# Optimization experiments

Hardware: AMD Instinct MI355X
Metric: run time of the kernel (lower is better)

The kernel has to match this reference:

```python
import jax, jax.numpy as jnp
import numpy as np

N_QUBITS = 12


def _apply_rx(state, q, theta, n):
    B = state.shape[0]
    left, right = 1 << q, 1 << (n - q - 1)
    s = state.reshape(B, left, 2, right)
    th = jnp.atleast_1d(jnp.asarray(theta)).reshape(-1, 1, 1)  # (B,1,1) or (1,1,1)
    c = jnp.cos(0.5 * th).astype(state.dtype)
    ms = (-1j * jnp.sin(0.5 * th)).astype(state.dtype)
    s0, s1 = s[:, :, 0, :], s[:, :, 1, :]
    new = jnp.stack([c * s0 + ms * s1, ms * s0 + c * s1], axis=2)
    return new.reshape(B, -1)


def _apply_cnot(state, ctrl, tgt, n):
    # flip target amplitudes on the control=1 slab
    B = state.shape[0]
    a, b = min(ctrl, tgt), max(ctrl, tgt)
    shape = (B, 1 << a, 2, 1 << (b - a - 1), 2, 1 << (n - b - 1))
    ax_c = 2 if ctrl == a else 4
    ax_t = 4 if ctrl == a else 2
    s = state.reshape(shape)
    s0 = jnp.take(s, 0, axis=ax_c)
    s1 = jnp.take(s, 1, axis=ax_c)
    ax_t_after = ax_t - 1 if ax_t > ax_c else ax_t
    s1 = jnp.flip(s1, axis=ax_t_after)
    return jnp.stack([s0, s1], axis=ax_c).reshape(B, -1)


def _simulate(x, w):
    # x: (B, n) angles; w: (L, n) angles. Returns (B, n) Pauli-Z expectations.
    B, n = x.shape
    L = w.shape[0]
    state = jnp.zeros((B, 1 << n), jnp.complex64).at[:, 0].set(1.0)
    # angle embedding: RX(x[:, j]) on qubit j
    for j in range(n):
        state = _apply_rx(state, j, x[:, j], n)
    # VQC layers: RX(w[i, j]) then ring of CNOTs
    for i in range(L):
        for j in range(n):
            state = _apply_rx(state, j, w[i, j], n)
        if n == 2:
            state = _apply_cnot(state, 0, 1, n)
        elif n > 2:
            for j in range(n):
                state = _apply_cnot(state, j, (j + 1) % n, n)
    probs = state.real ** 2 + state.imag ** 2  # (B, 2^n)
    exps = []
    for i in range(n):
        p = probs.reshape(B, 1 << i, 2, -1).sum(axis=(1, 3))  # (B, 2)
        exps.append(p[:, 0] - p[:, 1])
    return jnp.stack(exps, axis=-1)


def setup_inputs() -> dict:
    key = jax.random.key(0)
    k1, k2 = jax.random.split(key)
    x = jax.random.normal(k1, (2048, N_QUBITS), dtype=jnp.float32)
    # xavier_normal-ish init for w of shape (num_layers, num_qubits)
    w = jax.random.normal(k2, (2, N_QUBITS), dtype=jnp.float32) * 0.3
    return {"x": x, "w": w}


def reference(x, w):
    return _simulate(x, w)
```

## Files before the change

### kernel.cpp

```cpp
#include <hip/hip_runtime.h>

#define NQ 12
#define NSTATES (1 << NQ)

struct QPlan { unsigned rx2[NQ]; unsigned sgn[NQ]; };

constexpr QPlan make_plan() {
    QPlan P{};
    unsigned grow[NQ] = {}, hcol[NQ] = {};
    for (int j = 0; j < NQ; ++j) { grow[j] = 1u << j; hcol[j] = 1u << j; }
    for (int j = 0; j < NQ; ++j) {
        int cb = NQ - 1 - j, tb = NQ - 1 - ((j + 1) % NQ);
        grow[tb] ^= grow[cb]; hcol[cb] ^= hcol[tb];
    }
    for (int q = 0; q < NQ; ++q) P.rx2[q] = hcol[NQ - 1 - q];
    for (int j = 0; j < NQ; ++j) {
        int cb = NQ - 1 - j, tb = NQ - 1 - ((j + 1) % NQ);
        grow[tb] ^= grow[cb]; hcol[cb] ^= hcol[tb];
    }
    for (int q = 0; q < NQ; ++q) P.sgn[q] = grow[NQ - 1 - q];
    return P;
}
constexpr QPlan QP = make_plan();

__device__ __forceinline__ void rx_pair(float& ur, float& ui, float& vr, float& vi,
                                        float c, float s) {
    float nur = fmaf(c, ur,  s * vi);
    float nui = fmaf(c, ui, -s * vr);
    float nvr = fmaf(c, vr,  s * ui);
    float nvi = fmaf(c, vi, -s * ur);
    ur = nur; ui = nui; vr = nvr; vi = nvi;
}

template <int MLOC>
__device__ __forceinline__ void rx_local(float (&ar)[64], float (&ai)[64], float c, float s) {
    #pragma unroll
    for (int ka = 0; ka < 64; ++ka) {
        const int kb = ka ^ MLOC;
        if (ka < kb) rx_pair(ar[ka], ai[ka], ar[kb], ai[kb], c, s);
    }
}

template <int MLOC, int LM>
__device__ __forceinline__ void rx_shfl(float (&ar)[64], float (&ai)[64], float c, float s) {
    if constexpr (MLOC == 0) {
        #pragma unroll
        for (int k = 0; k < 64; ++k) {
            float pr = __shfl_xor(ar[k], LM, 64);
            float pi = __shfl_xor(ai[k], LM, 64);
            ar[k] = fmaf(c, ar[k],  s * pi);
            ai[k] = fmaf(c, ai[k], -s * pr);
        }
    } else {
        #pragma unroll
        for (int ka = 0; ka < 64; ++ka) {
            const int kb = ka ^ MLOC;
            if (ka < kb) {
                float pra = __shfl_xor(ar[kb], LM, 64);
                float pia = __shfl_xor(ai[kb], LM, 64);
                float prb = __shfl_xor(ar[ka], LM, 64);
                float pib = __shfl_xor(ai[ka], LM, 64);
                ar[ka] = fmaf(c, ar[ka],  s * pia);
                ai[ka] = fmaf(c, ai[ka], -s * pra);
                ar[kb] = fmaf(c, ar[kb],  s * pib);
                ai[kb] = fmaf(c, ai[kb], -s * prb);
            }
        }
    }
}

template <unsigned MASK>
__device__ __forceinline__ void rx_A(float (&ar)[64], float (&ai)[64], float c, float s) {
    constexpr int MLOC = MASK & 63, LM = (MASK >> 6) & 63;
    if constexpr (LM == 0) rx_local<MLOC>(ar, ai, c, s);
    else                   rx_shfl<MLOC, LM>(ar, ai, c, s);
}
template <unsigned MASK>
__device__ __forceinline__ void rx_B(float (&ar)[64], float (&ai)[64], float c, float s) {
    constexpr int MLOC = (MASK >> 6) & 63, LM = MASK & 63;
    if constexpr (LM == 0) rx_local<MLOC>(ar, ai, c, s);
    else                   rx_shfl<MLOC, LM>(ar, ai, c, s);
}

__global__ __launch_bounds__(64, 2) void qsim_fast(
    const float* __restrict__ x, const float* __restrict__ w, float* __restrict__ out)
{
    __shared__ float tbuf[64 * 65];
    const int b = blockIdx.x;
    const int l = threadIdx.x;

    float c0[NQ], s0[NQ], c2[NQ], s2[NQ];
    #pragma unroll
    for (int j = 0; j < NQ; ++j) {
        __sincosf(0.5f * (x[b * NQ + j] + w[j]), &s0[j], &c0[j]);
        __sincosf(0.5f * w[NQ + j],              &s2[j], &c2[j]);
    }

    float ar[64], ai[64];
    {
        float Flo[8], Fhi[8];
        #pragma unroll
        for (int a = 0; a < 8; ++a) {
            Flo[a] = ((a & 1) ? s0[5] : c0[5]) * ((a & 2) ? s0[4] : c0[4]) * ((a & 4) ? s0[3] : c0[3]);
            Fhi[a] = ((a & 1) ? s0[2] : c0[2]) * ((a & 2) ? s0[1] : c0[1]) * ((a & 4) ? s0[0] : c0[0]);
        }
        float Flane = ((l & 1)  ? s0[11] : c0[11]) * ((l & 2)  ? s0[10] : c0[10])
                    * ((l & 4)  ? s0[9]  : c0[9])  * ((l & 8)  ? s0[8]  : c0[8])
                    * ((l & 16) ? s0[7]  : c0[7])  * ((l & 32) ? s0[6]  : c0[6]);
        const int r = __popc(l);
        float rs[4], is[4];
        #pragma unroll
        for (int cc = 0; cc < 4; ++cc) {
            int n2 = (r + cc) & 3;
            rs[cc] = (n2 == 0) ? 1.f : ((n2 == 2) ? -1.f : 0.f);
            is[cc] = (n2 == 1) ? -1.f : ((n2 == 3) ? 1.f : 0.f);
        }
        #pragma unroll
        for (int k = 0; k < 64; ++k) {
            float m = Flane * Fhi[k >> 3] * Flo[k & 7];
            const int cls = __builtin_popcount((unsigned)k) & 3;
            ar[k] = m * rs[cls];
            ai[k] = m * is[cls];
        }
    }

    rx_B<QP.rx2[0]>(ar, ai, c2[0], s2[0]);
    rx_B<QP.rx2[1]>(ar, ai, c2[1], s2[1]);
    rx_B<QP.rx2[2]>(ar, ai, c2[2], s2[2]);
    rx_B<QP.rx2[3]>(ar, ai, c2[3], s2[3]);
    rx_B<QP.rx2[4]>(ar, ai, c2[4], s2[4]);

    #pragma unroll
    for (int k = 0; k < 64; ++k) tbuf[k * 65 + l] = ar[k];
    __syncthreads();
    #pragma unroll
    for (int k = 0; k < 64; ++k) ar[k] = tbuf[l * 65 + k];
    __syncthreads();
    #pragma unroll
    for (int k = 0; k < 64; ++k) tbuf[k * 65 + l] = ai[k];
    __syncthreads();
    #pragma unroll
    for (int k = 0; k < 64; ++k) ai[k] = tbuf[l * 65 + k];

    rx_A<QP.rx2[6]>(ar, ai, c2[6], s2[6]);
    rx_A<QP.rx2[7]>(ar, ai, c2[7], s2[7]);
    rx_A<QP.rx2[8]>(ar, ai, c2[8], s2[8]);
    rx_A<QP.rx2[9]>(ar, ai, c2[9], s2[9]);
    rx_A<QP.rx2[10]>(ar, ai, c2[10], s2[10]);
    rx_A<QP.rx2[5]>(ar, ai, c2[5], s2[5]);
    rx_A<QP.rx2[11]>(ar, ai, c2[11], s2[11]);

    float ex[NQ];
    #pragma unroll
    for (int q = 0; q < NQ; ++q) ex[q] = 0.f;
    #pragma unroll
    for (int k = 0; k < 64; ++k) {
        float p = fmaf(ar[k], ar[k], ai[k] * ai[k]);
        #pragma unroll
        for (int q = 0; q < NQ; ++q) {
            if (__builtin_popcount(QP.sgn[q] & (unsigned)k) & 1) ex[q] -= p;
            else                                                 ex[q] += p;
        }
    }
    #pragma unroll
    for (int q = 0; q < NQ; ++q) {
        float lsgn = (__popc(((QP.sgn[q] >> 6) & 63u) & (unsigned)l) & 1) ? -1.f : 1.f;
        float v = ex[q] * lsgn;
        #pragma unroll
        for (int off = 32; off >= 1; off >>= 1) v += __shfl_xor(v, off, 64);
        ex[q] = v;
    }
    float o = 0.f;
    #pragma unroll
    for (int q = 0; q < NQ; ++q) o = (l == q) ? ex[q] : o;
    if (l < NQ) out[b * NQ + l] = o;
}

__global__ __launch_bounds__(256) void qsim_generic(
    const float* __restrict__ x, const float* __restrict__ w,
    float* __restrict__ out, int L)
{
    __shared__ float re[NSTATES];
    __shared__ float im[NSTATES];
    __shared__ float wsum[4][NQ];
    const int b = blockIdx.x;
    const int t = threadIdx.x;

    for (int i = t; i < NSTATES; i += 256) { re[i] = 0.0f; im[i] = 0.0f; }
    if (t == 0) re[0] = 1.0f;
    __syncthreads();

    auto apply_rx = [&](int q, float theta) {
        const int bit = NQ - 1 - q, mask = 1 << bit;
        const float c = cosf(0.5f * theta), s = sinf(0.5f * theta);
        #pragma unroll
        for (int it = 0; it < NSTATES / 2 / 256; ++it) {
            const int p  = t + it * 256;
            const int i0 = ((p >> bit) << (bit + 1)) | (p & (mask - 1));
            const int i1 = i0 | mask;
            const float a0r = re[i0], a0i = im[i0], a1r = re[i1], a1i = im[i1];
            re[i0] = c * a0r + s * a1i;  im[i0] = c * a0i - s * a1r;
            re[i1] = c * a1r + s * a0i;  im[i1] = c * a1i - s * a0r;
        }
        __syncthreads();
    };
    auto apply_cnot = [&](int ctrl, int tgt) {
        const int cbit = NQ - 1 - ctrl, tbit = NQ - 1 - tgt;
        const int lo = cbit < tbit ? cbit : tbit, hi = cbit < tbit ? tbit : cbit;
        #pragma unroll
        for (int it = 0; it < NSTATES / 4 / 256; ++it) {
            const int p  = t + it * 256;
            const int x1 = ((p  >> lo) << (lo + 1)) | (p  & ((1 << lo) - 1));
            const int x2 = ((x1 >> hi) << (hi + 1)) | (x1 & ((1 << hi) - 1));
            const int ia = x2 | (1 << cbit), ib = ia | (1 << tbit);
            const float tr = re[ia]; re[ia] = re[ib]; re[ib] = tr;
            const float ti = im[ia]; im[ia] = im[ib]; im[ib] = ti;
        }
        __syncthreads();
    };

    for (int j = 0; j < NQ; ++j) apply_rx(j, x[b * NQ + j]);
    for (int l2 = 0; l2 < L; ++l2) {
        for (int j = 0; j < NQ; ++j) apply_rx(j, w[l2 * NQ + j]);
        for (int j = 0; j < NQ; ++j) apply_cnot(j, (j + 1) % NQ);
    }

    float ex[NQ];
    #pragma unroll
    for (int q = 0; q < NQ; ++q) ex[q] = 0.0f;
    #pragma unroll
    for (int it = 0; it < NSTATES / 256; ++it) {
        const int i = t + it * 256;
        const float p = re[i] * re[i] + im[i] * im[i];
        #pragma unroll
        for (int q = 0; q < NQ; ++q) ex[q] += ((i >> (NQ - 1 - q)) & 1) ? -p : p;
    }
    #pragma unroll
    for (int q = 0; q < NQ; ++q) {
        float v = ex[q];
        #pragma unroll
        for (int off = 32; off > 0; off >>= 1) v += __shfl_down(v, off, 64);
        ex[q] = v;
    }
    const int wid = t >> 6, lane = t & 63;
    if (lane == 0) {
        #pragma unroll
        for (int q = 0; q < NQ; ++q) wsum[wid][q] = ex[q];
    }
    __syncthreads();
    if (t < NQ) {
        float v = 0.0f;
        #pragma unroll
        for (int k = 0; k < 4; ++k) v += wsum[k][t];
        out[b * NQ + t] = v;
    }
}

extern "C" void kernel_launch(void* const* d_in, const int* in_sizes, int n_in,
                              void* d_out, int out_size, void* d_ws, size_t ws_size,
                              hipStream_t stream) {
    const float* x = (const float*)d_in[0];
    const float* w = (const float*)d_in[1];
    float* out = (float*)d_out;
    const int B = in_sizes[0] / NQ;
    const int L = in_sizes[1] / NQ;
    if (L == 2) {
        qsim_fast<<<dim3(B), dim3(64), 0, stream>>>(x, w, out);
    } else {
        qsim_generic<<<dim3(B), dim3(256), 0, stream>>>(x, w, out, L);
    }
}
```

Baseline: 70.97 us.

## Factor state into per-thread product and split across 256 threads with fewer gates

Result: faster. 69.23 us (-2.5%).

```diff
diff --git a/kernel.cpp b/kernel.cpp
--- a/kernel.cpp
+++ b/kernel.cpp
@@ -23,157 +23,190 @@
 }
 constexpr QPlan QP = make_plan();
 
-__device__ __forceinline__ void rx_pair(float& ur, float& ui, float& vr, float& vi,
-                                        float c, float s) {
-    float nur = fmaf(c, ur,  s * vi);
-    float nui = fmaf(c, ui, -s * vr);
-    float nvr = fmaf(c, vr,  s * ui);
-    float nvi = fmaf(c, vi, -s * ur);
-    ur = nur; ui = nui; vr = nvr; vi = nvi;
-}
-
-template <int MLOC>
-__device__ __forceinline__ void rx_local(float (&ar)[64], float (&ai)[64], float c, float s) {
-    #pragma unroll
-    for (int ka = 0; ka < 64; ++ka) {
-        const int kb = ka ^ MLOC;
-        if (ka < kb) rx_pair(ar[ka], ai[ka], ar[kb], ai[kb], c, s);
-    }
-}
-
-template <int MLOC, int LM>
-__device__ __forceinline__ void rx_shfl(float (&ar)[64], float (&ai)[64], float c, float s) {
-    if constexpr (MLOC == 0) {
-        #pragma unroll
-        for (int k = 0; k < 64; ++k) {
-            float pr = __shfl_xor(ar[k], LM, 64);
-            float pi = __shfl_xor(ai[k], LM, 64);
-            ar[k] = fmaf(c, ar[k],  s * pi);
-            ai[k] = fmaf(c, ai[k], -s * pr);
-        }
-    } else {
-        #pragma unroll
-        for (int ka = 0; ka < 64; ++ka) {
-            const int kb = ka ^ MLOC;
-            if (ka < kb) {
-                float pra = __shfl_xor(ar[kb], LM, 64);
-                float pia = __shfl_xor(ai[kb], LM, 64);
-                float prb = __shfl_xor(ar[ka], LM, 64);
-                float pib = __shfl_xor(ai[ka], LM, 64);
-                ar[ka] = fmaf(c, ar[ka],  s * pia);
-                ai[ka] = fmaf(c, ai[ka], -s * pra);
-                ar[kb] = fmaf(c, ar[kb],  s * pib);
-                ai[kb] = fmaf(c, ai[kb], -s * prb);
-            }
-        }
-    }
-}
-
-template <unsigned MASK>
-__device__ __forceinline__ void rx_A(float (&ar)[64], float (&ai)[64], float c, float s) {
-    constexpr int MLOC = MASK & 63, LM = (MASK >> 6) & 63;
-    if constexpr (LM == 0) rx_local<MLOC>(ar, ai, c, s);
-    else                   rx_shfl<MLOC, LM>(ar, ai, c, s);
-}
-template <unsigned MASK>
-__device__ __forceinline__ void rx_B(float (&ar)[64], float (&ai)[64], float c, float s) {
-    constexpr int MLOC = (MASK >> 6) & 63, LM = MASK & 63;
-    if constexpr (LM == 0) rx_local<MLOC>(ar, ai, c, s);
-    else                   rx_shfl<MLOC, LM>(ar, ai, c, s);
-}
-
-__global__ __launch_bounds__(64, 2) void qsim_fast(
+constexpr unsigned kpart(unsigned m) {
+    return ((m >> 0) & 1u) | (((m >> 9) & 1u) << 1) | (((m >> 10) & 1u) << 2) | (((m >> 11) & 1u) << 3);
+}
+constexpr unsigned lpart(unsigned m) {
+    return ((m >> 1) & 1u) | (((m >> 2) & 1u) << 1) | (((m >> 3) & 1u) << 2)
+         | (((m >> 6) & 1u) << 3) | (((m >> 7) & 1u) << 4) | (((m >> 8) & 1u) << 5);
+}
+constexpr unsigned wpart(unsigned m) {
+    return ((m >> 4) & 1u) | (((m >> 5) & 1u) << 1);
+}
+constexpr unsigned tpart(unsigned m) { return lpart(m) | (wpart(m) << 6); }
+
+static_assert(kpart(QP.rx2[0]) == 12 && tpart(QP.rx2[0]) == 0, "v-local");
+static_assert(kpart(QP.rx2[1]) == 6  && tpart(QP.rx2[1]) == 0, "v-local");
+static_assert(kpart(QP.rx2[11]) == 13 && tpart(QP.rx2[11]) == 0, "v-local triple");
+static_assert(kpart(QP.rx2[3]) == 0 && wpart(QP.rx2[3]) == 0 && lpart(QP.rx2[3]) == 48, "lane scalar");
+static_assert(kpart(QP.rx2[4]) == 0 && wpart(QP.rx2[4]) == 0 && lpart(QP.rx2[4]) == 24, "lane scalar");
+static_assert(kpart(QP.rx2[8]) == 0 && wpart(QP.rx2[8]) == 0 && lpart(QP.rx2[8]) == 6,  "lane scalar");
+static_assert(kpart(QP.rx2[9]) == 0 && wpart(QP.rx2[9]) == 0 && lpart(QP.rx2[9]) == 3,  "lane scalar");
+static_assert(kpart(QP.rx2[5]) == 0 && tpart(QP.rx2[5]) == 136, "cross scalar");
+static_assert(kpart(QP.rx2[6]) == 0 && tpart(QP.rx2[6]) == 192, "cross scalar");
+static_assert(kpart(QP.rx2[7]) == 0 && tpart(QP.rx2[7]) == 68,  "cross scalar");
+static_assert(kpart(QP.rx2[2]) == 2 && lpart(QP.rx2[2]) == 32 && wpart(QP.rx2[2]) == 0, "mixed");
+static_assert(kpart(QP.rx2[10]) == 1 && lpart(QP.rx2[10]) == 1 && wpart(QP.rx2[10]) == 0, "mixed");
+
+struct SignPlan { unsigned ks[NQ]; unsigned ts[NQ]; };
+constexpr SignPlan make_signs() {
+    SignPlan S{};
+    for (int q = 0; q < NQ; ++q) { S.ks[q] = kpart(QP.sgn[q]); S.ts[q] = tpart(QP.sgn[q]); }
+    return S;
+}
+constexpr SignPlan SP = make_signs();
+
+template <int KM>
+__device__ __forceinline__ void vgate(float (&vr)[16], float (&vi)[16], float c, float s) {
+    #pragma unroll
+    for (int ka = 0; ka < 16; ++ka) {
+        const int kb = ka ^ KM;
+        if (ka < kb) {
+            float nur = fmaf(c, vr[ka],  s * vi[kb]);
+            float nui = fmaf(c, vi[ka], -s * vr[kb]);
+            float nvr = fmaf(c, vr[kb],  s * vi[ka]);
+            float nvi = fmaf(c, vi[kb], -s * vr[ka]);
+            vr[ka] = nur; vi[ka] = nui; vr[kb] = nvr; vi[kb] = nvi;
+        }
+    }
+}
+
+template <int KM, int LM>
+__device__ __forceinline__ void mixed_gate(float (&ar)[16], float (&ai)[16], float c, float s) {
+    #pragma unroll
+    for (int ka = 0; ka < 16; ++ka) {
+        const int kb = ka ^ KM;
+        if (ka < kb) {
+            float pra = __shfl_xor(ar[kb], LM, 64);
+            float pia = __shfl_xor(ai[kb], LM, 64);
+            float prb = __shfl_xor(ar[ka], LM, 64);
+            float pib = __shfl_xor(ai[ka], LM, 64);
+            ar[ka] = fmaf(c, ar[ka],  s * pia);
+            ai[ka] = fmaf(c, ai[ka], -s * pra);
+            ar[kb] = fmaf(c, ar[kb],  s * pib);
+            ai[kb] = fmaf(c, ai[kb], -s * prb);
+        }
+    }
+}
+
+__global__ __launch_bounds__(256, 4) void qsim_fast(
     const float* __restrict__ x, const float* __restrict__ w, float* __restrict__ out)
 {
-    __shared__ float tbuf[64 * 65];
+    __shared__ float xr[256], xi[256];
+    __shared__ float red[4][NQ];
     const int b = blockIdx.x;
-    const int l = threadIdx.x;
-
-    float c0[NQ], s0[NQ], c2[NQ], s2[NQ];
-    #pragma unroll
-    for (int j = 0; j < NQ; ++j) {
-        __sincosf(0.5f * (x[b * NQ + j] + w[j]), &s0[j], &c0[j]);
-        __sincosf(0.5f * w[NQ + j],              &s2[j], &c2[j]);
-    }
-
-    float ar[64], ai[64];
+    const int tid = threadIdx.x;
+    const int lane = tid & 63;
+
+    constexpr int TQ[8] = {10, 9, 8, 5, 4, 3, 7, 6};
+    float F = 1.f;
+    #pragma unroll
+    for (int i = 0; i < 8; ++i) {
+        float a = x[b * NQ + TQ[i]] + w[TQ[i]];
+        float s, c; __sincosf(0.5f * a, &s, &c);
+        F *= ((tid >> i) & 1) ? s : c;
+    }
+    const int rt = __popc((unsigned)tid) & 3;
+    float sr = (rt == 0) ? F : (rt == 2 ? -F : 0.f);
+    float si = (rt == 1) ? -F : (rt == 3 ? F : 0.f);
+
+    constexpr int KQ[4] = {11, 2, 1, 0};
+    float kc[4], ks[4];
+    #pragma unroll
+    for (int i = 0; i < 4; ++i) {
+        float a = x[b * NQ + KQ[i]] + w[KQ[i]];
+        __sincosf(0.5f * a, &ks[i], &kc[i]);
+    }
+    float vr[16], vi[16];
+    #pragma unroll
+    for (int k = 0; k < 16; ++k) {
+        float g = ((k & 1) ? ks[0] : kc[0]) * ((k & 2) ? ks[1] : kc[1])
+                * ((k & 4) ? ks[2] : kc[2]) * ((k & 8) ? ks[3] : kc[3]);
+        const int rk = __builtin_popcount((unsigned)k) & 3;
+        vr[k] = (rk == 0) ? g : (rk == 2 ? -g : 0.f);
+        vi[k] = (rk == 1) ? -g : (rk == 3 ? g : 0.f);
+    }
+
     {
-        float Flo[8], Fhi[8];
-        #pragma unroll
-        for (int a = 0; a < 8; ++a) {
-            Flo[a] = ((a & 1) ? s0[5] : c0[5]) * ((a & 2) ? s0[4] : c0[4]) * ((a & 4) ? s0[3] : c0[3]);
-            Fhi[a] = ((a & 1) ? s0[2] : c0[2]) * ((a & 2) ? s0[1] : c0[1]) * ((a & 4) ? s0[0] : c0[0]);
-        }
-        float Flane = ((l & 1)  ? s0[11] : c0[11]) * ((l & 2)  ? s0[10] : c0[10])
-                    * ((l & 4)  ? s0[9]  : c0[9])  * ((l & 8)  ? s0[8]  : c0[8])
-                    * ((l & 16) ? s0[7]  : c0[7])  * ((l & 32) ? s0[6]  : c0[6]);
-        const int r = __popc(l);
-        float rs[4], is[4];
-        #pragma unroll
-        for (int cc = 0; cc < 4; ++cc) {
-            int n2 = (r + cc) & 3;
-            rs[cc] = (n2 == 0) ? 1.f : ((n2 == 2) ? -1.f : 0.f);
-            is[cc] = (n2 == 1) ? -1.f : ((n2 == 3) ? 1.f : 0.f);
-        }
-        #pragma unroll
-        for (int k = 0; k < 64; ++k) {
-            float m = Flane * Fhi[k >> 3] * Flo[k & 7];
-            const int cls = __builtin_popcount((unsigned)k) & 3;
-            ar[k] = m * rs[cls];
-            ai[k] = m * is[cls];
-        }
-    }
-
-    rx_B<QP.rx2[0]>(ar, ai, c2[0], s2[0]);
-    rx_B<QP.rx2[1]>(ar, ai, c2[1], s2[1]);
-    rx_B<QP.rx2[2]>(ar, ai, c2[2], s2[2]);
-    rx_B<QP.rx2[3]>(ar, ai, c2[3], s2[3]);
-    rx_B<QP.rx2[4]>(ar, ai, c2[4], s2[4]);
-
-    #pragma unroll
-    for (int k = 0; k < 64; ++k) tbuf[k * 65 + l] = ar[k];
-    __syncthreads();
-    #pragma unroll
-    for (int k = 0; k < 64; ++k) ar[k] = tbuf[l * 65 + k];
-    __syncthreads();
-    #pragma unroll
-    for (int k = 0; k < 64; ++k) tbuf[k * 65 + l] = ai[k];
-    __syncthreads();
-    #pragma unroll
-    for (int k = 0; k < 64; ++k) ai[k] = tbuf[l * 65 + k];
-
-    rx_A<QP.rx2[6]>(ar, ai, c2[6], s2[6]);
-    rx_A<QP.rx2[7]>(ar, ai, c2[7], s2[7]);
-    rx_A<QP.rx2[8]>(ar, ai, c2[8], s2[8]);
-    rx_A<QP.rx2[9]>(ar, ai, c2[9], s2[9]);
-    rx_A<QP.rx2[10]>(ar, ai, c2[10], s2[10]);
-    rx_A<QP.rx2[5]>(ar, ai, c2[5], s2[5]);
-    rx_A<QP.rx2[11]>(ar, ai, c2[11], s2[11]);
+        float s, c;
+        __sincosf(0.5f * w[NQ + 0],  &s, &c); vgate<12>(vr, vi, c, s);
+        __sincosf(0.5f * w[NQ + 1],  &s, &c); vgate<6>(vr, vi, c, s);
+        __sincosf(0.5f * w[NQ + 11], &s, &c); vgate<13>(vr, vi, c, s);
+    }
+
+    {
+        const int LMs[4] = {48, 24, 6, 3};
+        const int JJ[4]  = {3, 4, 8, 9};
+        #pragma unroll
+        for (int i = 0; i < 4; ++i) {
+            float s, c; __sincosf(0.5f * w[NQ + JJ[i]], &s, &c);
+            float pr = __shfl_xor(sr, LMs[i], 64);
+            float pi = __shfl_xor(si, LMs[i], 64);
+            sr = fmaf(c, sr,  s * pi);
+            si = fmaf(c, si, -s * pr);
+        }
+    }
+
+    {
+        float s5, c5, s6, c6, s7, c7;
+        __sincosf(0.5f * w[NQ + 5], &s5, &c5);
+        __sincosf(0.5f * w[NQ + 6], &s6, &c6);
+        __sincosf(0.5f * w[NQ + 7], &s7, &c7);
+        xr[tid] = sr; xi[tid] = si;
+        __syncthreads();
+        const float m0 = c5 * c6 * c7;
+        const float m5 = s5 * c6 * c7, m6 = c5 * s6 * c7, m7 = c5 * c6 * s7;
+        const float m56 = s5 * s6 * c7, m57 = s5 * c6 * s7, m67 = c5 * s6 * s7;
+        const float m567 = s5 * s6 * s7;
+        float nr = m0 * sr, ni = m0 * si;
+        { float pr = xr[tid ^ 136], pi = xi[tid ^ 136]; nr = fmaf( m5, pi, nr); ni = fmaf(-m5, pr, ni); }
+        { float pr = xr[tid ^ 192], pi = xi[tid ^ 192]; nr = fmaf( m6, pi, nr); ni = fmaf(-m6, pr, ni); }
+        { float pr = xr[tid ^  68], pi = xi[tid ^  68]; nr = fmaf( m7, pi, nr); ni = fmaf(-m7, pr, ni); }
+        { float pr = xr[tid ^  72], pi = xi[tid ^  72]; nr = fmaf(-m56, pr, nr); ni = fmaf(-m56, pi, ni); }
+        { float pr = xr[tid ^ 204], pi = xi[tid ^ 204]; nr = fmaf(-m57, pr, nr); ni = fmaf(-m57, pi, ni); }
+        { float pr = xr[tid ^ 132], pi = xi[tid ^ 132]; nr = fmaf(-m67, pr, nr); ni = fmaf(-m67, pi, ni); }
+        { float pr = xr[tid ^  12], pi = xi[tid ^  12]; nr = fmaf(-m567, pi, nr); ni = fmaf( m567, pr, ni); }
+        sr = nr; si = ni;
+    }
+
+    float ar[16], ai[16];
+    #pragma unroll
+    for (int k = 0; k < 16; ++k) {
+        ar[k] = sr * vr[k] - si * vi[k];
+        ai[k] = sr * vi[k] + si * vr[k];
+    }
+    {
+        float s, c;
+        __sincosf(0.5f * w[NQ + 2],  &s, &c); mixed_gate<2, 32>(ar, ai, c, s);
+        __sincosf(0.5f * w[NQ + 10], &s, &c); mixed_gate<1, 1>(ar, ai, c, s);
+    }
 
     float ex[NQ];
     #pragma unroll
     for (int q = 0; q < NQ; ++q) ex[q] = 0.f;
     #pragma unroll
-    for (int k = 0; k < 64; ++k) {
-        float p = fmaf(ar[k], ar[k], ai[k] * ai[k]);
+    for (int k = 0; k < 16; ++k) {
+        float p2 = fmaf(ar[k], ar[k], ai[k] * ai[k]);
         #pragma unroll
         for (int q = 0; q < NQ; ++q) {
-            if (__builtin_popcount(QP.sgn[q] & (unsigned)k) & 1) ex[q] -= p;
-            else                                                 ex[q] += p;
+            if (__builtin_popcount(SP.ks[q] & (unsigned)k) & 1) ex[q] -= p2;
+            else                                                ex[q] += p2;
         }
     }
     #pragma unroll
     for (int q = 0; q < NQ; ++q) {
-        float lsgn = (__popc(((QP.sgn[q] >> 6) & 63u) & (unsigned)l) & 1) ? -1.f : 1.f;
-        float v = ex[q] * lsgn;
+        float v = (__popc(SP.ts[q] & (unsigned)tid) & 1) ? -ex[q] : ex[q];
         #pragma unroll
         for (int off = 32; off >= 1; off >>= 1) v += __shfl_xor(v, off, 64);
         ex[q] = v;
     }
+    const int wv = tid >> 6;
     float o = 0.f;
     #pragma unroll
-    for (int q = 0; q < NQ; ++q) o = (l == q) ? ex[q] : o;
-    if (l < NQ) out[b * NQ + l] = o;
+    for (int q = 0; q < NQ; ++q) o = (lane == q) ? ex[q] : o;
+    if (lane < NQ) red[wv][lane] = o;
+    __syncthreads();
+    if (tid < NQ) out[b * NQ + tid] = red[0][tid] + red[1][tid] + red[2][tid] + red[3][tid];
 }
 
 __global__ __launch_bounds__(256) void qsim_generic(
@@ -265,7 +298,7 @@
     const int B = in_sizes[0] / NQ;
     const int L = in_sizes[1] / NQ;
     if (L == 2) {
-        qsim_fast<<<dim3(B), dim3(64), 0, stream>>>(x, w, out);
+        qsim_fast<<<dim3(B), dim3(256), 0, stream>>>(x, w, out);
     } else {
         qsim_generic<<<dim3(B), dim3(256), 0, stream>>>(x, w, out, L);
     }
```
